# Optimization experiments

Hardware: AMD Instinct MI355X
Metric: run time of the kernel (lower is better)

## Reference

```python
import jax, jax.numpy as jnp
import numpy as np

B, S, HID = 2, 2048, 4096
H, KVH, D = 32, 8, 128
THETA = 10000.0
SCALE = D ** -0.5


def _rope(x, positions):
    # x: [B, S, nH, D], positions: [B, S] int. Neox style: rotate halves.
    half = D // 2
    inv_freq = 1.0 / (THETA ** (jnp.arange(0, half, dtype=jnp.float32) / half))
    ang = positions.astype(jnp.float32)[..., None] * inv_freq  # [B,S,half]
    cos = jnp.cos(ang)[:, :, None, :]  # [B,S,1,half]
    sin = jnp.sin(ang)[:, :, None, :]
    x1, x2 = x[..., :half], x[..., half:]
    return jnp.concatenate([x1 * cos - x2 * sin, x2 * cos + x1 * sin], axis=-1)


def setup_inputs() -> dict:
    key = jax.random.key(0)
    k1, k2, k3, k4, k5 = jax.random.split(key, 5)
    std_in = HID ** -0.5
    return {
        "positions": jnp.tile(jnp.arange(S, dtype=jnp.int32), (B, 1)),
        "hidden_states": jax.random.normal(k1, (B, S, HID), jnp.float32),
        "wq": jax.random.normal(k2, (HID, H * D), jnp.float32) * std_in,
        "wk": jax.random.normal(k3, (HID, KVH * D), jnp.float32) * std_in,
        "wv": jax.random.normal(k4, (HID, KVH * D), jnp.float32) * std_in,
        "wo": jax.random.normal(k5, (H * D, HID), jnp.float32) * ((H * D) ** -0.5),
    }


def reference(positions, hidden_states, wq, wk, wv, wo):
    # Separate Q/K/V projections (bias=False)
    q = (hidden_states @ wq).reshape(B, S, H, D)
    k = (hidden_states @ wk).reshape(B, S, KVH, D)
    v = (hidden_states @ wv).reshape(B, S, KVH, D)
    # RoPE on q and k
    q = _rope(q, positions)
    k = _rope(k, positions)
    # GQA: expand KV heads to query heads
    group = H // KVH
    k = jnp.repeat(k, group, axis=2)  # [B,S,H,D]
    v = jnp.repeat(v, group, axis=2)
    # Causal scaled dot-product attention
    scores = jnp.einsum("bqhd,bkhd->bhqk", q, k) * SCALE
    causal = jnp.tril(jnp.ones((S, S), dtype=bool))
    scores = jnp.where(causal, scores, jnp.finfo(scores.dtype).min)
    probs = jax.nn.softmax(scores, axis=-1)
    attn = jnp.einsum("bhqk,bkhd->bqhd", probs, v).reshape(B, S, H * D)
    return attn @ wo
```

## Files before the change

kernel.cpp:

```cpp
#include <hip/hip_runtime.h>
#include <cstdint>

typedef __bf16 bf16;
typedef __attribute__((ext_vector_type(4))) __bf16 bf16x4;
typedef __attribute__((ext_vector_type(8))) __bf16 bf16x8;
typedef __attribute__((ext_vector_type(4))) float f32x4;

#define DEVI __device__ __forceinline__

#define BATCH 2
#define SEQ 2048
#define HID 4096
#define NH 32
#define NKVH 8
#define HD 128
#define QKVN 6144
#define MROWS 4096
#define ATT_SCALE 0.08838834764831845f
#define QSCALE (0.08838834764831845f * 1.4426950408889634f)

DEVI void gload_lds16(const bf16* g, bf16* l) {
  __builtin_amdgcn_global_load_lds(
      (__attribute__((address_space(1))) void*)(g),
      (__attribute__((address_space(3))) void*)(l), 16, 0, 0);
}

__global__ void h2b_kernel(const float* __restrict__ in, bf16* __restrict__ out) {
  long i = ((long)blockIdx.x * 256 + threadIdx.x) * 4;
  float4 v = *(const float4*)(in + i);
  bf16x4 o;
  o[0] = (bf16)v.x; o[1] = (bf16)v.y; o[2] = (bf16)v.z; o[3] = (bf16)v.w;
  *(bf16x4*)(out + i) = o;
}

__global__ void wtrans_kernel(const float* __restrict__ in, bf16* __restrict__ out,
                              int K, int N) {
  __shared__ float t[32][33];
  int n0 = blockIdx.x * 32, k0 = blockIdx.y * 32;
  int tx = threadIdx.x, ty = threadIdx.y;
#pragma unroll
  for (int r = 0; r < 4; ++r) {
    int k = ty + r * 8;
    t[k][tx] = in[(long)(k0 + k) * N + n0 + tx];
  }
  __syncthreads();
#pragma unroll
  for (int r = 0; r < 4; ++r) {
    int n = ty + r * 8;
    out[(long)(n0 + n) * K + k0 + tx] = (bf16)t[tx][n];
  }
}

__global__ void rope_kernel(bf16* __restrict__ qkv, const int* __restrict__ pos) {
  long idx = (long)blockIdx.x * 256 + threadIdx.x;
  if (idx >= (long)MROWS * 40 * 64) return;
  int d = idx & 63;
  long t = idx >> 6;
  int hh = (int)(t % 40);
  int row = (int)(t / 40);
  int colb = hh < NH ? hh * HD : NH * HD + (hh - NH) * HD;
  float p = (float)pos[row];
  float inv_freq = exp2f((float)d * -0.2076205059304601f);
  float ang = p * inv_freq;
  float sn = sinf(ang), cs = cosf(ang);
  bf16* base = qkv + (long)row * QKVN + colb + d;
  float x1 = (float)base[0], x2 = (float)base[64];
  base[0] = (bf16)(x1 * cs - x2 * sn);
  base[64] = (bf16)(x2 * cs + x1 * sn);
}

__global__ void vtrans_kernel(const bf16* __restrict__ qkv, bf16* __restrict__ vt) {
  __shared__ bf16 t[32][33];
  int s0 = blockIdx.x * 32, d0 = blockIdx.y * 32, bk = blockIdx.z;
  int b = bk >> 3, kvh = bk & 7;
  int tx = threadIdx.x, ty = threadIdx.y;
#pragma unroll
  for (int r = 0; r < 4; ++r) {
    int s = ty + r * 8;
    t[s][tx] = qkv[(long)(b * SEQ + s0 + s) * QKVN + 5120 + kvh * HD + d0 + tx];
  }
  __syncthreads();
#pragma unroll
  for (int r = 0; r < 4; ++r) {
    int d = ty + r * 8;
    vt[((long)bk * HD + d0 + d) * SEQ + s0 + tx] = t[tx][d];
  }
}

template <typename OutT>
__global__ __launch_bounds__(512, 2)
void gemm256(const bf16* __restrict__ A, const bf16* __restrict__ BT,
             OutT* __restrict__ C, int M, int N, int K) {
  extern __shared__ __align__(16) bf16 lds[];
  const int tid = threadIdx.x;
  const int lane = tid & 63, wave = tid >> 6;
  const int wm = wave >> 1, wn = wave & 1;
  const int l16 = lane & 15, lhi = lane >> 4;
  const int nwg = gridDim.x * gridDim.y;
  const int bid = blockIdx.y * gridDim.x + blockIdx.x;
  const int cpx = nwg >> 3;
  const int swz = (bid & 7) * cpx + (bid >> 3);
  const int bx = swz % gridDim.x, by = swz / gridDim.x;
  const long bm0 = (long)by * 256, bn0 = (long)bx * 128;

  const int srow8 = lane >> 3;
  const int scol = (lane & 7) ^ srow8;

  const int NT = K >> 6;
  f32x4 acc[4][4] = {};

  auto stage = [&](int slot, int t) {
    const long k0 = (long)t << 6;
    bf16* dst = lds + slot * 24576;
#pragma unroll
    for (int i = 0; i < 4; ++i) {
      int r = (wave * 4 + i) * 8 + srow8;
      gload_lds16(A + (bm0 + r) * K + k0 + scol * 8,
                  dst + (wave * 4 + i) * 512 + lane * 8);
    }
#pragma unroll
    for (int i = 0; i < 2; ++i) {
      int r = (wave * 2 + i) * 8 + srow8;
      gload_lds16(BT + (bn0 + r) * K + k0 + scol * 8,
                  dst + 16384 + (wave * 2 + i) * 512 + lane * 8);
    }
  };

  stage(0, 0);
  stage(1, 1);

  for (int t = 0; t < NT; ++t) {
    asm volatile("s_waitcnt vmcnt(6)" ::: "memory");
    __builtin_amdgcn_s_barrier();
    __builtin_amdgcn_sched_barrier(0);
    const int nxt = (t + 2 < NT) ? t + 2 : NT - 1;
    stage((t + 2) % 3, nxt);
    const bf16* As = lds + (t % 3) * 24576;
    const bf16* Bs = As + 16384;
#pragma unroll
    for (int kk = 0; kk < 2; ++kk) {
      bf16x8 af[4], bw[4];
#pragma unroll
      for (int i = 0; i < 4; ++i) {
        int ar = wm * 64 + i * 16 + l16;
        af[i] = *(const bf16x8*)(As + ar * 64 + (((kk * 4 + lhi) ^ (ar & 7))) * 8);
        int br = wn * 64 + i * 16 + l16;
        bw[i] = *(const bf16x8*)(Bs + br * 64 + (((kk * 4 + lhi) ^ (br & 7))) * 8);
      }
      __builtin_amdgcn_s_setprio(1);
#pragma unroll
      for (int i = 0; i < 4; ++i)
#pragma unroll
        for (int j = 0; j < 4; ++j)
          acc[i][j] = __builtin_amdgcn_mfma_f32_16x16x32_bf16(af[i], bw[j], acc[i][j], 0, 0, 0);
      __builtin_amdgcn_s_setprio(0);
    }
  }
  asm volatile("s_waitcnt vmcnt(0)" ::: "memory");
#pragma unroll
  for (int i = 0; i < 4; ++i)
#pragma unroll
    for (int r = 0; r < 4; ++r) {
      long grow = bm0 + wm * 64 + i * 16 + lhi * 4 + r;
#pragma unroll
      for (int j = 0; j < 4; ++j) {
        long gcol = bn0 + wn * 64 + j * 16 + l16;
        C[grow * N + gcol] = (OutT)acc[i][j][r];
      }
    }
}

__global__ __launch_bounds__(512, 4)
void attn_kernel(const bf16* __restrict__ qkv, const bf16* __restrict__ vt,
                 bf16* __restrict__ out) {
  extern __shared__ __align__(16) bf16 smem[];
  const int pi = blockIdx.x, h = blockIdx.y, b = blockIdx.z;
  const int kvh = h >> 2;
  const int tid = threadIdx.x, lane = tid & 63, wave = tid >> 6;
  const int l16 = lane & 15, lhi = lane >> 4;
  const int kloc = lhi * 4;
  bf16* Pw = smem + 32768 + wave * 1024;

  const bf16* kpan = qkv + (long)(b * SEQ) * QKVN + 4096 + kvh * HD;
  const bf16* vpan = vt + (long)(b * NKVH + kvh) * HD * SEQ;

  auto stageKV = [&](int buf, int step) {
    const int kv0 = step * 64;
    bf16* kd = smem + buf * 8192;
    bf16* vd = smem + 16384 + buf * 8192;
#pragma unroll
    for (int i = 0; i < 2; ++i) {
      int kr = wave * 8 + i * 4 + lhi;
      gload_lds16(kpan + (long)(kv0 + kr) * QKVN + (l16 ^ (kr & 7)) * 8,
                  kd + (wave * 8 + i * 4) * 128);
      int vr = wave * 16 + i * 8 + (lane >> 3);
      gload_lds16(vpan + (long)vr * SEQ + kv0 + ((lane & 7) ^ (vr & 7)) * 8,
                  vd + (wave * 16 + i * 8) * 64);
    }
  };

  auto process_chunk = [&](int q0, int nsteps) {
    bf16x8 qf[4];
    const bf16* qb = qkv + (long)(b * SEQ + q0 + wave * 16 + l16) * QKVN + h * HD + lhi * 8;
#pragma unroll
    for (int di = 0; di < 4; ++di) {
      bf16x8 raw = *(const bf16x8*)(qb + di * 32);
      bf16x8 sc;
#pragma unroll
      for (int j = 0; j < 8; ++j) sc[j] = (bf16)((float)raw[j] * QSCALE);
      qf[di] = sc;
    }
    f32x4 oacc[8] = {};
    float m_run = -1e30f, l_run = 0.f;
    const int qg = q0 + wave * 16 + l16;

    stageKV(0, 0);
    __syncthreads();

    for (int step = 0; step < nsteps; ++step) {
      const int kv0 = step * 64;
      const int cur = step & 1;
      if (step + 1 < nsteps) stageKV(cur ^ 1, step + 1);
      const bf16* Kc = smem + cur * 8192;
      const bf16* Vc = smem + 16384 + cur * 8192;

      f32x4 s[4];
      __builtin_amdgcn_s_setprio(1);
#pragma unroll
      for (int c = 0; c < 4; ++c) {
        s[c] = (f32x4){0.f, 0.f, 0.f, 0.f};
        int kr = c * 16 + l16;
#pragma unroll
        for (int di = 0; di < 4; ++di) {
          bf16x8 kf = *(const bf16x8*)(Kc + kr * 128 + (((di * 4 + lhi) ^ (kr & 7))) * 8);
          s[c] = __builtin_amdgcn_mfma_f32_16x16x32_bf16(kf, qf[di], s[c], 0, 0, 0);
        }
      }
      __builtin_amdgcn_s_setprio(0);
#pragma unroll
      for (int c = 0; c < 4; ++c)
#pragma unroll
        for (int r = 0; r < 4; ++r) {
          int kcol = kv0 + c * 16 + kloc + r;
          if (kcol > qg) s[c][r] = -1e30f;
        }
      float mloc = s[0][0];
#pragma unroll
      for (int c = 0; c < 4; ++c)
#pragma unroll
        for (int r = 0; r < 4; ++r) mloc = fmaxf(mloc, s[c][r]);
      mloc = fmaxf(mloc, __shfl_xor(mloc, 16, 64));
      mloc = fmaxf(mloc, __shfl_xor(mloc, 32, 64));
      bool skip = __all(mloc - m_run <= 8.0f);
      float alpha = 1.f;
      if (!skip) {
        float mn = fmaxf(m_run, mloc);
        alpha = exp2f(m_run - mn);
        m_run = mn;
      }
      float sm = 0.f;
      bf16x4 pb[4];
#pragma unroll
      for (int c = 0; c < 4; ++c)
#pragma unroll
        for (int r = 0; r < 4; ++r) {
          float p = exp2f(s[c][r] - m_run);
          sm += p;
          pb[c][r] = (bf16)p;
        }
      sm += __shfl_xor(sm, 16, 64);
      sm += __shfl_xor(sm, 32, 64);
      l_run = l_run * alpha + sm;
#pragma unroll
      for (int c = 0; c < 4; ++c) {
        int sl = (c * 2 + (lhi >> 1)) ^ (l16 & 7);
        *(bf16x4*)(Pw + l16 * 64 + sl * 8 + (lhi & 1) * 4) = pb[c];
      }
      if (!skip) {
        float a_o[4];
#pragma unroll
        for (int r = 0; r < 4; ++r) a_o[r] = __shfl(alpha, kloc + r, 64);
#pragma unroll
        for (int dj = 0; dj < 8; ++dj)
#pragma unroll
          for (int r = 0; r < 4; ++r) oacc[dj][r] *= a_o[r];
      }
      __builtin_amdgcn_s_setprio(1);
#pragma unroll
      for (int kh = 0; kh < 2; ++kh) {
        bf16x8 pf = *(const bf16x8*)(Pw + l16 * 64 + (((kh * 4 + lhi) ^ (l16 & 7))) * 8);
#pragma unroll
        for (int dj = 0; dj < 8; ++dj) {
          int vr = dj * 16 + l16;
          bf16x8 vf = *(const bf16x8*)(Vc + vr * 64 + (((kh * 4 + lhi) ^ (vr & 7))) * 8);
          oacc[dj] = __builtin_amdgcn_mfma_f32_16x16x32_bf16(pf, vf, oacc[dj], 0, 0, 0);
        }
      }
      __builtin_amdgcn_s_setprio(0);
      __syncthreads();
    }
    float linv[4];
#pragma unroll
    for (int r = 0; r < 4; ++r) linv[r] = 1.f / __shfl(l_run, kloc + r, 64);
#pragma unroll
    for (int r = 0; r < 4; ++r) {
      long orow = (long)(b * SEQ + q0 + wave * 16 + lhi * 4 + r);
#pragma unroll
      for (int dj = 0; dj < 8; ++dj)
        out[orow * (NH * HD) + h * HD + dj * 16 + l16] = (bf16)(oacc[dj][r] * linv[r]);
    }
  };

  process_chunk(pi * 128, 2 * pi + 2);
  process_chunk((15 - pi) * 128, 32 - 2 * pi);
}

extern "C" void kernel_launch(void* const* d_in, const int* in_sizes, int n_in,
                              void* d_out, int out_size, void* d_ws, size_t ws_size,
                              hipStream_t stream) {
  const int* positions = (const int*)d_in[0];
  const float* hidden = (const float*)d_in[1];
  const float* wq = (const float*)d_in[2];
  const float* wk = (const float*)d_in[3];
  const float* wv = (const float*)d_in[4];
  const float* wo = (const float*)d_in[5];
  float* out = (float*)d_out;
  char* ws = (char*)d_ws;

  const size_t SZ_H = (size_t)MROWS * HID * 2;
  const size_t SZ_WQKV = (size_t)QKVN * HID * 2;
  const size_t SZ_WO = (size_t)HID * HID * 2;
  bf16* h_bf = (bf16*)(ws);
  bf16* wqkvT = (bf16*)(ws + SZ_H);
  bf16* woT = (bf16*)(ws + SZ_H + SZ_WQKV);
  bf16* qkv = (bf16*)(ws + SZ_H + SZ_WQKV + SZ_WO);
  bf16* attn = h_bf;
  bf16* vtbuf = wqkvT;

  const int GEMM_SMEM = 3 * 24576 * 2;
  const int ATTN_SMEM = 40960 * 2;
  auto* g1 = gemm256<bf16>;
  auto* g2 = gemm256<float>;
  hipFuncSetAttribute(reinterpret_cast<const void*>(g1),
                      hipFuncAttributeMaxDynamicSharedMemorySize, GEMM_SMEM);
  hipFuncSetAttribute(reinterpret_cast<const void*>(g2),
                      hipFuncAttributeMaxDynamicSharedMemorySize, GEMM_SMEM);
  hipFuncSetAttribute(reinterpret_cast<const void*>(attn_kernel),
                      hipFuncAttributeMaxDynamicSharedMemorySize, ATTN_SMEM);

  h2b_kernel<<<(MROWS * (long)HID) / (256 * 4), 256, 0, stream>>>(hidden, h_bf);
  dim3 t32(32, 8);
  wtrans_kernel<<<dim3(HID / 32, HID / 32), t32, 0, stream>>>(wq, wqkvT, HID, HID);
  wtrans_kernel<<<dim3(1024 / 32, HID / 32), t32, 0, stream>>>(wk, wqkvT + (long)4096 * HID, HID, 1024);
  wtrans_kernel<<<dim3(1024 / 32, HID / 32), t32, 0, stream>>>(wv, wqkvT + (long)5120 * HID, HID, 1024);
  wtrans_kernel<<<dim3(HID / 32, HID / 32), t32, 0, stream>>>(wo, woT, HID, HID);
  gemm256<bf16><<<dim3(QKVN / 128, MROWS / 256), 512, GEMM_SMEM, stream>>>(h_bf, wqkvT, qkv, MROWS, QKVN, HID);
  rope_kernel<<<(MROWS * 40 * 64) / 256, 256, 0, stream>>>(qkv, positions);
  vtrans_kernel<<<dim3(SEQ / 32, HD / 32, BATCH * NKVH), t32, 0, stream>>>(qkv, vtbuf);
  attn_kernel<<<dim3(8, NH, BATCH), 512, ATTN_SMEM, stream>>>(qkv, vtbuf, attn);
  gemm256<float><<<dim3(HID / 128, MROWS / 256), 512, GEMM_SMEM, stream>>>(attn, woT, out, MROWS, HID, HID);
}
```

Baseline: 554.9 us.

## Replace GEMM with 256x256 tile, 8-phase interleaved load/MFMA pipeline

Rewrites both projection GEMMs to use 256x256 output tiles with 8 waves in a 2x4 arrangement. K is double-buffered in 128 KB of LDS, and each K step is split into four MFMA quadrants. Global-to-LDS loads of half-tiles and LDS fragment reads are interleaved between barriers so memory traffic overlaps compute. The larger tile raises arithmetic intensity and cuts redundant A/B loads. In exchange it uses more registers and LDS, has fewer workgroups (e.g. 16x16=256 for the output GEMM), and adds many barriers per iteration.

```diff
diff --git a/kernel.cpp b/kernel.cpp
--- a/kernel.cpp
+++ b/kernel.cpp
@@ -89,83 +89,164 @@
 
 template <typename OutT>
 __global__ __launch_bounds__(512, 2)
-void gemm256(const bf16* __restrict__ A, const bf16* __restrict__ BT,
-             OutT* __restrict__ C, int M, int N, int K) {
+void gemm8p(const bf16* __restrict__ A, const bf16* __restrict__ BT,
+            OutT* __restrict__ C, int M, int N, int K) {
   extern __shared__ __align__(16) bf16 lds[];
   const int tid = threadIdx.x;
   const int lane = tid & 63, wave = tid >> 6;
-  const int wm = wave >> 1, wn = wave & 1;
+  const int wm = wave >> 2, wn = wave & 3;
   const int l16 = lane & 15, lhi = lane >> 4;
   const int nwg = gridDim.x * gridDim.y;
   const int bid = blockIdx.y * gridDim.x + blockIdx.x;
   const int cpx = nwg >> 3;
   const int swz = (bid & 7) * cpx + (bid >> 3);
   const int bx = swz % gridDim.x, by = swz / gridDim.x;
-  const long bm0 = (long)by * 256, bn0 = (long)bx * 128;
-
-  const int srow8 = lane >> 3;
-  const int scol = (lane & 7) ^ srow8;
-
+  const long bm0 = (long)by * 256, bn0 = (long)bx * 256;
+
+  bf16* Alds = lds;
+  bf16* Blds = lds + 32768;
   const int NT = K >> 6;
-  f32x4 acc[4][4] = {};
-
-  auto stage = [&](int slot, int t) {
-    const long k0 = (long)t << 6;
-    bf16* dst = lds + slot * 24576;
+
+  f32x4 acc[8][4] = {};
+
+  auto stageH = [&](const bf16* src, long row0, long k0, bf16* dst) {
+#pragma unroll
+    for (int j = 0; j < 2; ++j) {
+      int r = j * 64 + (tid >> 3);
+      int sc = (tid & 7) ^ (r & 7);
+      gload_lds16(src + (row0 + r) * (long)K + k0 + sc * 8,
+                  dst + j * 4096 + tid * 8);
+    }
+  };
+
+  stageH(A, bm0, 0, Alds);
+  stageH(A, bm0 + 128, 0, Alds + 8192);
+  stageH(BT, bn0, 0, Blds);
+  stageH(BT, bn0 + 128, 0, Blds + 8192);
+  {
+    long k1 = (NT > 1) ? 64 : 0;
+    stageH(BT, bn0, k1, Blds + 16384);
+    stageH(BT, bn0 + 128, k1, Blds + 24576);
+    stageH(A, bm0, k1, Alds + 16384);
+  }
+  asm volatile("s_waitcnt vmcnt(6)" ::: "memory");
+  __builtin_amdgcn_s_barrier();
+  __builtin_amdgcn_sched_barrier(0);
+
+  const int arow0 = wm * 128 + l16;
+  const int brow0 = wn * 64 + l16;
+
+  for (int t = 0; t < NT; ++t) {
+    const bf16* Ab = Alds + (t & 1) * 16384;
+    const bf16* Bb = Blds + (t & 1) * 16384;
+    bf16* A1 = Alds + ((t + 1) & 1) * 16384;
+    bf16* A2 = Alds + (t & 1) * 16384;
+    bf16* B2 = Blds + (t & 1) * 16384;
+    const long k1 = (long)((t + 1 < NT) ? t + 1 : NT - 1) << 6;
+    const long k2 = (long)((t + 2 < NT) ? t + 2 : NT - 1) << 6;
+
+    bf16x8 a0[4][2], a1r[4][2], b0[2][2], b1[2][2];
 #pragma unroll
     for (int i = 0; i < 4; ++i) {
-      int r = (wave * 4 + i) * 8 + srow8;
-      gload_lds16(A + (bm0 + r) * K + k0 + scol * 8,
-                  dst + (wave * 4 + i) * 512 + lane * 8);
-    }
-#pragma unroll
-    for (int i = 0; i < 2; ++i) {
-      int r = (wave * 2 + i) * 8 + srow8;
-      gload_lds16(BT + (bn0 + r) * K + k0 + scol * 8,
-                  dst + 16384 + (wave * 2 + i) * 512 + lane * 8);
-    }
-  };
-
-  stage(0, 0);
-  stage(1, 1);
-
-  for (int t = 0; t < NT; ++t) {
+      int mr = arow0 + i * 16;
+#pragma unroll
+      for (int kk = 0; kk < 2; ++kk)
+        a0[i][kk] = *(const bf16x8*)(Ab + mr * 64 + (((kk * 4 + lhi) ^ (mr & 7))) * 8);
+    }
+#pragma unroll
+    for (int n = 0; n < 2; ++n) {
+      int br = brow0 + n * 16;
+#pragma unroll
+      for (int kk = 0; kk < 2; ++kk)
+        b0[n][kk] = *(const bf16x8*)(Bb + br * 64 + (((kk * 4 + lhi) ^ (br & 7))) * 8);
+    }
+    stageH(A, bm0 + 128, k1, A1 + 8192);
+    __builtin_amdgcn_sched_barrier(0);
+    __builtin_amdgcn_s_barrier();
+    __builtin_amdgcn_sched_barrier(0);
+    __builtin_amdgcn_s_setprio(1);
+#pragma unroll
+    for (int i = 0; i < 4; ++i)
+#pragma unroll
+      for (int n = 0; n < 2; ++n)
+#pragma unroll
+        for (int kk = 0; kk < 2; ++kk)
+          acc[i][n] = __builtin_amdgcn_mfma_f32_16x16x32_bf16(a0[i][kk], b0[n][kk], acc[i][n], 0, 0, 0);
+    __builtin_amdgcn_s_setprio(0);
+    __builtin_amdgcn_sched_barrier(0);
+    __builtin_amdgcn_s_barrier();
+#pragma unroll
+    for (int n = 0; n < 2; ++n) {
+      int br = brow0 + (n + 2) * 16;
+#pragma unroll
+      for (int kk = 0; kk < 2; ++kk)
+        b1[n][kk] = *(const bf16x8*)(Bb + br * 64 + (((kk * 4 + lhi) ^ (br & 7))) * 8);
+    }
+    __builtin_amdgcn_sched_barrier(0);
+    __builtin_amdgcn_s_barrier();
+    __builtin_amdgcn_sched_barrier(0);
+    __builtin_amdgcn_s_setprio(1);
+#pragma unroll
+    for (int i = 0; i < 4; ++i)
+#pragma unroll
+      for (int n = 0; n < 2; ++n)
+#pragma unroll
+        for (int kk = 0; kk < 2; ++kk)
+          acc[i][n + 2] = __builtin_amdgcn_mfma_f32_16x16x32_bf16(a0[i][kk], b1[n][kk], acc[i][n + 2], 0, 0, 0);
+    __builtin_amdgcn_s_setprio(0);
+    __builtin_amdgcn_sched_barrier(0);
+    __builtin_amdgcn_s_barrier();
+#pragma unroll
+    for (int i = 0; i < 4; ++i) {
+      int mr = arow0 + 64 + i * 16;
+#pragma unroll
+      for (int kk = 0; kk < 2; ++kk)
+        a1r[i][kk] = *(const bf16x8*)(Ab + mr * 64 + (((kk * 4 + lhi) ^ (mr & 7))) * 8);
+    }
+    stageH(BT, bn0, k2, B2);
+    __builtin_amdgcn_sched_barrier(0);
+    __builtin_amdgcn_s_barrier();
+    __builtin_amdgcn_sched_barrier(0);
+    __builtin_amdgcn_s_setprio(1);
+#pragma unroll
+    for (int i = 0; i < 4; ++i)
+#pragma unroll
+      for (int n = 0; n < 2; ++n)
+#pragma unroll
+        for (int kk = 0; kk < 2; ++kk)
+          acc[4 + i][n + 2] = __builtin_amdgcn_mfma_f32_16x16x32_bf16(a1r[i][kk], b1[n][kk], acc[4 + i][n + 2], 0, 0, 0);
+    __builtin_amdgcn_s_setprio(0);
+    __builtin_amdgcn_sched_barrier(0);
+    __builtin_amdgcn_s_barrier();
+    stageH(BT, bn0 + 128, k2, B2 + 8192);
+    stageH(A, bm0, k2, A2);
+    __builtin_amdgcn_sched_barrier(0);
+    __builtin_amdgcn_s_barrier();
+    __builtin_amdgcn_sched_barrier(0);
+    __builtin_amdgcn_s_setprio(1);
+#pragma unroll
+    for (int i = 0; i < 4; ++i)
+#pragma unroll
+      for (int n = 0; n < 2; ++n)
+#pragma unroll
+        for (int kk = 0; kk < 2; ++kk)
+          acc[4 + i][n] = __builtin_amdgcn_mfma_f32_16x16x32_bf16(a1r[i][kk], b0[n][kk], acc[4 + i][n], 0, 0, 0);
+    __builtin_amdgcn_s_setprio(0);
+    __builtin_amdgcn_sched_barrier(0);
     asm volatile("s_waitcnt vmcnt(6)" ::: "memory");
     __builtin_amdgcn_s_barrier();
     __builtin_amdgcn_sched_barrier(0);
-    const int nxt = (t + 2 < NT) ? t + 2 : NT - 1;
-    stage((t + 2) % 3, nxt);
-    const bf16* As = lds + (t % 3) * 24576;
-    const bf16* Bs = As + 16384;
-#pragma unroll
-    for (int kk = 0; kk < 2; ++kk) {
-      bf16x8 af[4], bw[4];
-#pragma unroll
-      for (int i = 0; i < 4; ++i) {
-        int ar = wm * 64 + i * 16 + l16;
-        af[i] = *(const bf16x8*)(As + ar * 64 + (((kk * 4 + lhi) ^ (ar & 7))) * 8);
-        int br = wn * 64 + i * 16 + l16;
-        bw[i] = *(const bf16x8*)(Bs + br * 64 + (((kk * 4 + lhi) ^ (br & 7))) * 8);
-      }
-      __builtin_amdgcn_s_setprio(1);
-#pragma unroll
-      for (int i = 0; i < 4; ++i)
-#pragma unroll
-        for (int j = 0; j < 4; ++j)
-          acc[i][j] = __builtin_amdgcn_mfma_f32_16x16x32_bf16(af[i], bw[j], acc[i][j], 0, 0, 0);
-      __builtin_amdgcn_s_setprio(0);
-    }
   }
   asm volatile("s_waitcnt vmcnt(0)" ::: "memory");
 #pragma unroll
-  for (int i = 0; i < 4; ++i)
+  for (int mi = 0; mi < 8; ++mi)
 #pragma unroll
     for (int r = 0; r < 4; ++r) {
-      long grow = bm0 + wm * 64 + i * 16 + lhi * 4 + r;
-#pragma unroll
-      for (int j = 0; j < 4; ++j) {
-        long gcol = bn0 + wn * 64 + j * 16 + l16;
-        C[grow * N + gcol] = (OutT)acc[i][j][r];
+      long grow = bm0 + wm * 128 + mi * 16 + lhi * 4 + r;
+#pragma unroll
+      for (int n = 0; n < 4; ++n) {
+        long gcol = bn0 + wn * 64 + n * 16 + l16;
+        C[grow * N + gcol] = (OutT)acc[mi][n][r];
       }
     }
 }
@@ -337,10 +418,10 @@
   bf16* attn = h_bf;
   bf16* vtbuf = wqkvT;
 
-  const int GEMM_SMEM = 3 * 24576 * 2;
+  const int GEMM_SMEM = 131072;
   const int ATTN_SMEM = 40960 * 2;
-  auto* g1 = gemm256<bf16>;
-  auto* g2 = gemm256<float>;
+  auto* g1 = gemm8p<bf16>;
+  auto* g2 = gemm8p<float>;
   hipFuncSetAttribute(reinterpret_cast<const void*>(g1),
                       hipFuncAttributeMaxDynamicSharedMemorySize, GEMM_SMEM);
   hipFuncSetAttribute(reinterpret_cast<const void*>(g2),
@@ -354,9 +435,9 @@
   wtrans_kernel<<<dim3(1024 / 32, HID / 32), t32, 0, stream>>>(wk, wqkvT + (long)4096 * HID, HID, 1024);
   wtrans_kernel<<<dim3(1024 / 32, HID / 32), t32, 0, stream>>>(wv, wqkvT + (long)5120 * HID, HID, 1024);
   wtrans_kernel<<<dim3(HID / 32, HID / 32), t32, 0, stream>>>(wo, woT, HID, HID);
-  gemm256<bf16><<<dim3(QKVN / 128, MROWS / 256), 512, GEMM_SMEM, stream>>>(h_bf, wqkvT, qkv, MROWS, QKVN, HID);
+  gemm8p<bf16><<<dim3(QKVN / 256, MROWS / 256), 512, GEMM_SMEM, stream>>>(h_bf, wqkvT, qkv, MROWS, QKVN, HID);
   rope_kernel<<<(MROWS * 40 * 64) / 256, 256, 0, stream>>>(qkv, positions);
   vtrans_kernel<<<dim3(SEQ / 32, HD / 32, BATCH * NKVH), t32, 0, stream>>>(qkv, vtbuf);
   attn_kernel<<<dim3(8, NH, BATCH), 512, ATTN_SMEM, stream>>>(qkv, vtbuf, attn);
-  gemm256<float><<<dim3(HID / 128, MROWS / 256), 512, GEMM_SMEM, stream>>>(attn, woT, out, MROWS, HID, HID);
-}
+  gemm8p<float><<<dim3(HID / 256, MROWS / 256), 512, GEMM_SMEM, stream>>>(attn, woT, out, MROWS, HID, HID);
+}
```

After: 553.3 us. Within noise of the previous version (-0.3%).
